# Kernel tuning notes

Hardware: AMD Instinct MI355X
Metric: run time of the kernel (lower is better)

Reference implementation:

```python
import jax, jax.numpy as jnp
import numpy as np

HEADS = 4
DIM_HEAD = 64


def setup_inputs() -> dict:
    key = jax.random.key(0)
    k1, k2, k3, k4 = jax.random.split(key, 4)
    dim = 256
    hidden = HEADS * DIM_HEAD  # 256
    x = jax.random.normal(k1, (16, dim, 64, 64), dtype=jnp.float32)
    # 1x1 conv weights stored as [out_c, in_c]
    w_qkv = jax.random.normal(k2, (3 * hidden, dim), dtype=jnp.float32) * (1.0 / np.sqrt(dim))
    w_out = jax.random.normal(k3, (dim, hidden), dtype=jnp.float32) * (1.0 / np.sqrt(hidden))
    b_out = jax.random.normal(k4, (dim,), dtype=jnp.float32) * 0.01
    gamma = jnp.ones((dim,), dtype=jnp.float32) * 1e-05
    return {"x": x, "w_qkv": w_qkv, "w_out": w_out, "b_out": b_out, "gamma": gamma}


def reference(x, w_qkv, w_out, b_out, gamma):
    b, c, h, w = x.shape
    n = h * w
    # 1x1 conv == channel matmul
    qkv = jnp.einsum('oc,bchw->bohw', w_qkv, x)  # [b, 3*heads*dh, h, w]
    qkv = qkv.reshape(b, 3, HEADS, DIM_HEAD, n)  # channel split order: (qkv, heads, c)
    q, k, v = qkv[:, 0], qkv[:, 1], qkv[:, 2]    # each [b, heads, dh, n]
    k = jax.nn.softmax(k, axis=-1)               # softmax over spatial tokens
    context = jnp.einsum('bhdn,bhen->bhde', k, v)  # [b, heads, dh, dh]
    out = jnp.einsum('bhde,bhdn->bhen', context, q)  # [b, heads, dh, n]
    out = out.reshape(b, HEADS * DIM_HEAD, h, w)
    y = jnp.einsum('oc,bchw->bohw', w_out, out) + b_out[None, :, None, None]
    return y * gamma[None, :, None, None] + x
```

## Files before the change

### kernel.cpp

```cpp
#include <hip/hip_runtime.h>
#include <stdint.h>

typedef short s16x8 __attribute__((ext_vector_type(8)));
typedef float f32x4 __attribute__((ext_vector_type(4)));

__device__ __forceinline__ float bits2f(unsigned short u) {
    union { unsigned int i; float f; } c; c.i = ((unsigned int)u) << 16; return c.f;
}
__device__ __forceinline__ unsigned short f2bits(float f) {
    union { float f; unsigned int i; } c; c.f = f;
    unsigned int x = c.i;
    unsigned int r = (x + 0x7FFFu + ((x >> 16) & 1u)) >> 16;
    return (unsigned short)r;
}
__device__ __forceinline__ unsigned int pack2(float a, float b) {
    return (unsigned int)f2bits(a) | ((unsigned int)f2bits(b) << 16);
}

__global__ __launch_bounds__(256) void k_cvt(
    const float* __restrict__ src, unsigned short* __restrict__ dst, int n8)
{
    int i = blockIdx.x * 256 + threadIdx.x;
    if (i >= n8) return;
    const float* s = src + (size_t)i * 8;
    float4 a = *(const float4*)s, b = *(const float4*)(s + 4);
    unsigned int q[4] = { pack2(a.x, a.y), pack2(a.z, a.w), pack2(b.x, b.y), pack2(b.z, b.w) };
    *(s16x8*)(dst + (size_t)i * 8) = *(s16x8*)q;
}

__global__ __launch_bounds__(256) void k_transpose(
    const unsigned short* __restrict__ src, unsigned short* __restrict__ dst,
    int RS, int DS)
{
    int dr = blockIdx.x * 256 + threadIdx.x;
    int c0 = blockIdx.y * 8;
    __align__(16) unsigned short tmp[8];
#pragma unroll
    for (int j = 0; j < 8; ++j) tmp[j] = src[(size_t)(c0 + j) * RS + dr];
    *(s16x8*)(dst + (size_t)dr * DS + c0) = *(s16x8*)tmp;
}

template <int EPI, int BBF16, int XCVT>
__global__ __launch_bounds__(256) void gemm_wide(
    const unsigned short* __restrict__ A, const void* __restrict__ B,
    void* __restrict__ C, unsigned short* __restrict__ xbout,
    const float* __restrict__ Xres, const float* __restrict__ gamma,
    const float* __restrict__ bias, long Abs)
{
    __shared__ unsigned short As[256][72];
    __shared__ unsigned short Bs[64][66];
    int bz = blockIdx.z;
    int n0 = blockIdx.x * 64;
    const unsigned short* Ab = A + (size_t)bz * Abs;
    int t = threadIdx.x, w = t >> 6, l = t & 63, lm = l & 15, lq = l >> 4;
    int mw = w * 64;

    f32x4 acc[4][4];
    f32x4 zero = {0.f, 0.f, 0.f, 0.f};
#pragma unroll
    for (int i = 0; i < 4; ++i)
#pragma unroll
        for (int j = 0; j < 4; ++j) acc[i][j] = zero;

    for (int kk = 0; kk < 256; kk += 64) {
#pragma unroll
        for (int i = 0; i < 8; ++i) {
            int idx = t + i * 256;
            int r = idx >> 3, ch = idx & 7;
            *(s16x8*)&As[r][ch * 8] = *(const s16x8*)(Ab + (size_t)r * 256 + kk + ch * 8);
        }
#pragma unroll
        for (int i = 0; i < 2; ++i) {
            int idx = t + i * 256;
            int c = idx >> 3, ch = idx & 7;
            unsigned int* qp = (unsigned int*)&Bs[c][ch * 8];
            if (BBF16) {
                const unsigned short* bp = (const unsigned short*)B + (size_t)bz * 1048576
                                         + (size_t)(kk + c) * 4096 + n0 + ch * 8;
                union { s16x8 v; unsigned int u[4]; } cv;
                cv.v = *(const s16x8*)bp;
                qp[0] = cv.u[0]; qp[1] = cv.u[1]; qp[2] = cv.u[2]; qp[3] = cv.u[3];
            } else {
                const float* bp = (const float*)B + (size_t)bz * 1048576
                                + (size_t)(kk + c) * 4096 + n0 + ch * 8;
                float4 v0 = *(const float4*)bp, v1 = *(const float4*)(bp + 4);
                unsigned int q[4] = { pack2(v0.x, v0.y), pack2(v0.z, v0.w),
                                      pack2(v1.x, v1.y), pack2(v1.z, v1.w) };
                qp[0] = q[0]; qp[1] = q[1]; qp[2] = q[2]; qp[3] = q[3];
                if (XCVT) {
                    unsigned short* xp = xbout + (size_t)bz * 1048576
                                       + (size_t)(kk + c) * 4096 + n0 + ch * 8;
                    *(s16x8*)xp = *(s16x8*)q;
                }
            }
        }
        __syncthreads();
#pragma unroll
        for (int ks = 0; ks < 2; ++ks) {
            s16x8 af[4];
#pragma unroll
            for (int mi = 0; mi < 4; ++mi)
                af[mi] = *(const s16x8*)&As[mw + mi * 16 + lm][ks * 32 + lq * 8];
#pragma unroll
            for (int ni = 0; ni < 4; ++ni) {
                s16x8 bfr;
#pragma unroll
                for (int j = 0; j < 8; ++j) bfr[j] = (short)Bs[ks * 32 + lq * 8 + j][ni * 16 + lm];
#pragma unroll
                for (int mi = 0; mi < 4; ++mi)
                    acc[mi][ni] = __builtin_amdgcn_mfma_f32_16x16x32_bf16(af[mi], bfr, acc[mi][ni], 0, 0, 0);
            }
        }
        __syncthreads();
    }

#pragma unroll
    for (int mi = 0; mi < 4; ++mi)
#pragma unroll
        for (int r = 0; r < 4; ++r) {
            int m = mw + mi * 16 + lq * 4 + r;
            float g = 0.f, bo = 0.f;
            if (EPI == 1) { g = gamma[m]; bo = bias[m]; }
#pragma unroll
            for (int ni = 0; ni < 4; ++ni) {
                int n = n0 + ni * 16 + lm;
                size_t idx = (size_t)m * 4096 + n;
                float v = acc[mi][ni][r];
                if (EPI == 1) {
                    float* Cb = (float*)C + (size_t)bz * 1048576;
                    Cb[idx] = g * (v + bo) + Xres[(size_t)bz * 1048576 + idx];
                } else {
                    unsigned short* Cb = (unsigned short*)C + (size_t)bz * 1048576;
                    Cb[idx] = f2bits(v);
                }
            }
        }
}

template <int AEXP>
__global__ __launch_bounds__(256) void gemm_bt(
    const unsigned short* __restrict__ A, const unsigned short* __restrict__ Bt,
    unsigned short* __restrict__ C, const float2* __restrict__ stats,
    int K, int Kstep, int lda, int ldb, int ldc,
    long Abs, long Bbs, long Cbs)
{
    __shared__ unsigned short As[128][72];
    __shared__ unsigned short Bs[128][72];
    int bz = blockIdx.z;
    int b = bz & 15, kc = bz >> 4;
    int m0 = blockIdx.y * 128, n0 = blockIdx.x * 128;
    const unsigned short* Ab = A + (size_t)b * Abs + (size_t)m0 * lda + (size_t)kc * Kstep;
    const unsigned short* Bb = Bt + (size_t)b * Bbs + (size_t)n0 * ldb + (size_t)kc * Kstep;
    int t = threadIdx.x;
    int w = t >> 6, l = t & 63, lm = l & 15, lq = l >> 4;
    int mw = (w >> 1) * 64, nw = (w & 1) * 64;

    f32x4 acc[4][4];
    f32x4 zero = {0.f, 0.f, 0.f, 0.f};
#pragma unroll
    for (int i = 0; i < 4; ++i)
#pragma unroll
        for (int j = 0; j < 4; ++j) acc[i][j] = zero;

    for (int kk = 0; kk < K; kk += 64) {
#pragma unroll
        for (int i = 0; i < 4; ++i) {
            int idx = t + i * 256;
            int r = idx >> 3, ch = idx & 7;
            s16x8 av = *(const s16x8*)(Ab + (size_t)r * lda + kk + ch * 8);
            if (AEXP) {
                float2 st = stats[b * 256 + m0 + r];
                unsigned int q[4];
#pragma unroll
                for (int j = 0; j < 4; ++j) {
                    float e0 = __expf(bits2f((unsigned short)av[2 * j]) - st.x) * st.y;
                    float e1 = __expf(bits2f((unsigned short)av[2 * j + 1]) - st.x) * st.y;
                    q[j] = pack2(e0, e1);
                }
                av = *(s16x8*)q;
            }
            *(s16x8*)&As[r][ch * 8] = av;
            *(s16x8*)&Bs[r][ch * 8] = *(const s16x8*)(Bb + (size_t)r * ldb + kk + ch * 8);
        }
        __syncthreads();
#pragma unroll
        for (int ks = 0; ks < 2; ++ks) {
            s16x8 af[4], bfr[4];
#pragma unroll
            for (int mi = 0; mi < 4; ++mi) af[mi]  = *(const s16x8*)&As[mw + mi * 16 + lm][ks * 32 + lq * 8];
#pragma unroll
            for (int ni = 0; ni < 4; ++ni) bfr[ni] = *(const s16x8*)&Bs[nw + ni * 16 + lm][ks * 32 + lq * 8];
#pragma unroll
            for (int mi = 0; mi < 4; ++mi)
#pragma unroll
                for (int ni = 0; ni < 4; ++ni)
                    acc[mi][ni] = __builtin_amdgcn_mfma_f32_16x16x32_bf16(af[mi], bfr[ni], acc[mi][ni], 0, 0, 0);
        }
        __syncthreads();
    }

    unsigned short* Cb = C + (size_t)bz * Cbs;
#pragma unroll
    for (int mi = 0; mi < 4; ++mi)
#pragma unroll
        for (int r = 0; r < 4; ++r) {
            int m = m0 + mw + mi * 16 + lq * 4 + r;
#pragma unroll
            for (int ni = 0; ni < 4; ++ni) {
                int n = n0 + nw + ni * 16 + lm;
                Cb[(size_t)m * ldc + n] = f2bits(acc[mi][ni][r]);
            }
        }
}

__global__ __launch_bounds__(256) void k_softstats(
    const unsigned short* __restrict__ kbuf, float2* __restrict__ stats)
{
    const unsigned short* p = kbuf + (size_t)blockIdx.x * 4096;
    int t = threadIdx.x;
    __shared__ float red[4];

    s16x8 r0 = *(const s16x8*)(p + t * 16);
    s16x8 r1 = *(const s16x8*)(p + t * 16 + 8);
    float v[16];
    float m = -1e30f;
#pragma unroll
    for (int i = 0; i < 8; ++i) { v[i] = bits2f((unsigned short)r0[i]); v[8 + i] = bits2f((unsigned short)r1[i]); }
#pragma unroll
    for (int i = 0; i < 16; ++i) m = fmaxf(m, v[i]);
#pragma unroll
    for (int off = 32; off >= 1; off >>= 1) m = fmaxf(m, __shfl_xor(m, off));
    if ((t & 63) == 0) red[t >> 6] = m;
    __syncthreads();
    m = fmaxf(fmaxf(red[0], red[1]), fmaxf(red[2], red[3]));
    __syncthreads();

    float s = 0.f;
#pragma unroll
    for (int i = 0; i < 16; ++i) s += __expf(v[i] - m);
#pragma unroll
    for (int off = 32; off >= 1; off >>= 1) s += __shfl_xor(s, off);
    if ((t & 63) == 0) red[t >> 6] = s;
    __syncthreads();
    if (t == 0) {
        s = red[0] + red[1] + red[2] + red[3];
        stats[blockIdx.x] = make_float2(m, 1.0f / s);
    }
}

__global__ __launch_bounds__(256) void k_ctxw2(
    const unsigned short* __restrict__ Gp, const unsigned short* __restrict__ wb,
    const unsigned short* __restrict__ wob, unsigned short* __restrict__ W2)
{
    __shared__ unsigned short ctxs[64][72];
    int h = blockIdx.x, b = blockIdx.y;
    int t = threadIdx.x, w = t >> 6, l = t & 63, lm = l & 15, lq = l >> 4;
    const unsigned short* Wv = wb + 131072 + (size_t)(h * 64) * 256;
    f32x4 zero = {0.f, 0.f, 0.f, 0.f};

    f32x4 acc[4];
#pragma unroll
    for (int i = 0; i < 4; ++i) acc[i] = zero;
    for (int kc = 0; kc < 8; ++kc) {
        const unsigned short* Gb = Gp + (size_t)(kc * 16 + b) * 65536 + (size_t)(h * 64) * 256;
#pragma unroll
        for (int kk = 0; kk < 256; kk += 32) {
            s16x8 a = *(const s16x8*)(Gb + (size_t)(w * 16 + lm) * 256 + kk + lq * 8);
#pragma unroll
            for (int ni = 0; ni < 4; ++ni) {
                s16x8 bb = *(const s16x8*)(Wv + (size_t)(ni * 16 + lm) * 256 + kk + lq * 8);
                acc[ni] = __builtin_amdgcn_mfma_f32_16x16x32_bf16(a, bb, acc[ni], 0, 0, 0);
            }
        }
    }
#pragma unroll
    for (int ni = 0; ni < 4; ++ni)
#pragma unroll
        for (int r = 0; r < 4; ++r)
            ctxs[w * 16 + lq * 4 + r][ni * 16 + lm] = f2bits(acc[ni][r]);
    __syncthreads();

    f32x4 acc2[4][4];
#pragma unroll
    for (int i = 0; i < 4; ++i)
#pragma unroll
        for (int j = 0; j < 4; ++j) acc2[i][j] = zero;
#pragma unroll
    for (int ks = 0; ks < 2; ++ks) {
        s16x8 af[4], bfr[4];
#pragma unroll
        for (int mi = 0; mi < 4; ++mi)
            af[mi] = *(const s16x8*)(wob + (size_t)(w * 64 + mi * 16 + lm) * 256 + h * 64 + ks * 32 + lq * 8);
#pragma unroll
        for (int ni = 0; ni < 4; ++ni) bfr[ni] = *(const s16x8*)&ctxs[ni * 16 + lm][ks * 32 + lq * 8];
#pragma unroll
        for (int mi = 0; mi < 4; ++mi)
#pragma unroll
            for (int ni = 0; ni < 4; ++ni)
                acc2[mi][ni] = __builtin_amdgcn_mfma_f32_16x16x32_bf16(af[mi], bfr[ni], acc2[mi][ni], 0, 0, 0);
    }
    unsigned short* W2b = W2 + (size_t)b * 65536;
#pragma unroll
    for (int mi = 0; mi < 4; ++mi)
#pragma unroll
        for (int r = 0; r < 4; ++r) {
            int o = w * 64 + mi * 16 + lq * 4 + r;
#pragma unroll
            for (int ni = 0; ni < 4; ++ni)
                W2b[(size_t)o * 256 + h * 64 + ni * 16 + lm] = f2bits(acc2[mi][ni][r]);
        }
}

extern "C" void kernel_launch(void* const* d_in, const int* in_sizes, int n_in,
                              void* d_out, int out_size, void* d_ws, size_t ws_size,
                              hipStream_t stream)
{
    (void)in_sizes; (void)n_in; (void)out_size; (void)ws_size;
    const float* x      = (const float*)d_in[0];
    const float* w_qkv  = (const float*)d_in[1];
    const float* w_out  = (const float*)d_in[2];
    const float* b_out  = (const float*)d_in[3];
    const float* gamma  = (const float*)d_in[4];
    unsigned short* kbuf = (unsigned short*)d_out;

    char* ws = (char*)d_ws;
    unsigned short* xb  = (unsigned short*)(ws);
    unsigned short* Gp  = (unsigned short*)(ws + 33554432);
    unsigned short* W2  = (unsigned short*)(ws + 50331648);
    unsigned short* W3  = (unsigned short*)(ws + 52428800);
    unsigned short* WqT = (unsigned short*)(ws + 54525952);
    unsigned short* wb  = (unsigned short*)(ws + 54657024);
    unsigned short* wob = (unsigned short*)(ws + 55050240);
    float2*         st  = (float2*)        (ws + 55181312);

    k_cvt<<<dim3(96), 256, 0, stream>>>(w_qkv, wb, 24576);
    k_cvt<<<dim3(32), 256, 0, stream>>>(w_out, wob, 8192);
    k_transpose<<<dim3(1, 32, 1), 256, 0, stream>>>(wb, WqT, 256, 256);

    gemm_wide<0, 0, 1><<<dim3(64, 1, 16), 256, 0, stream>>>(
        wb + 65536, x, kbuf, xb, nullptr, nullptr, nullptr, 0L);

    k_softstats<<<dim3(4096), 256, 0, stream>>>(kbuf, st);

    gemm_bt<1><<<dim3(2, 2, 128), 256, 0, stream>>>(
        kbuf, xb, Gp, st, 512, 512, 4096, 4096, 256,
        1048576L, 1048576L, 65536L);

    k_ctxw2<<<dim3(4, 16), 256, 0, stream>>>(Gp, wb, wob, W2);

    gemm_bt<0><<<dim3(2, 2, 16), 256, 0, stream>>>(
        W2, WqT, W3, nullptr, 256, 0, 256, 256, 256,
        65536L, 0L, 65536L);

    gemm_wide<1, 1, 0><<<dim3(64, 1, 16), 256, 0, stream>>>(
        W3, xb, d_out, nullptr, x, gamma, b_out, 65536L);
}
```

Measured before the change: 239.9 us.

## Replace wide GEMMs with transposed-x gemm_bt and fuse softmax sum into epilogue

Adds a kernel that converts x to bf16 and also writes a transposed [n, c] copy, so the key projection and the output projection can both run through the 128x128 gemm_bt kernel instead of the gemm_wide kernel with its strided shared-memory B reads. The separate softmax statistics pass is dropped: the key GEMM epilogue accumulates row sums of exp(k) with atomics, and the next GEMM normalises using only that sum, with no max subtraction. The weight conversion and transpose kernels are merged into one launch. The cost is an extra 32 MB transposed write and atomic traffic, plus a risk of exp overflow without the max shift, which is safe only while k stays bounded.

Result: no change. 237.9 us (-0.8%).

```diff
diff --git a/kernel.cpp b/kernel.cpp
--- a/kernel.cpp
+++ b/kernel.cpp
@@ -17,132 +17,77 @@
     return (unsigned int)f2bits(a) | ((unsigned int)f2bits(b) << 16);
 }
 
-__global__ __launch_bounds__(256) void k_cvt(
-    const float* __restrict__ src, unsigned short* __restrict__ dst, int n8)
+__global__ __launch_bounds__(256) void k_zero(float* __restrict__ p, int n)
 {
     int i = blockIdx.x * 256 + threadIdx.x;
-    if (i >= n8) return;
-    const float* s = src + (size_t)i * 8;
-    float4 a = *(const float4*)s, b = *(const float4*)(s + 4);
-    unsigned int q[4] = { pack2(a.x, a.y), pack2(a.z, a.w), pack2(b.x, b.y), pack2(b.z, b.w) };
-    *(s16x8*)(dst + (size_t)i * 8) = *(s16x8*)q;
-}
-
-__global__ __launch_bounds__(256) void k_transpose(
-    const unsigned short* __restrict__ src, unsigned short* __restrict__ dst,
-    int RS, int DS)
-{
-    int dr = blockIdx.x * 256 + threadIdx.x;
-    int c0 = blockIdx.y * 8;
-    __align__(16) unsigned short tmp[8];
-#pragma unroll
-    for (int j = 0; j < 8; ++j) tmp[j] = src[(size_t)(c0 + j) * RS + dr];
-    *(s16x8*)(dst + (size_t)dr * DS + c0) = *(s16x8*)tmp;
-}
-
-template <int EPI, int BBF16, int XCVT>
-__global__ __launch_bounds__(256) void gemm_wide(
-    const unsigned short* __restrict__ A, const void* __restrict__ B,
-    void* __restrict__ C, unsigned short* __restrict__ xbout,
-    const float* __restrict__ Xres, const float* __restrict__ gamma,
-    const float* __restrict__ bias, long Abs)
-{
-    __shared__ unsigned short As[256][72];
-    __shared__ unsigned short Bs[64][66];
-    int bz = blockIdx.z;
-    int n0 = blockIdx.x * 64;
-    const unsigned short* Ab = A + (size_t)bz * Abs;
-    int t = threadIdx.x, w = t >> 6, l = t & 63, lm = l & 15, lq = l >> 4;
-    int mw = w * 64;
-
-    f32x4 acc[4][4];
-    f32x4 zero = {0.f, 0.f, 0.f, 0.f};
-#pragma unroll
-    for (int i = 0; i < 4; ++i)
-#pragma unroll
-        for (int j = 0; j < 4; ++j) acc[i][j] = zero;
-
-    for (int kk = 0; kk < 256; kk += 64) {
-#pragma unroll
-        for (int i = 0; i < 8; ++i) {
-            int idx = t + i * 256;
-            int r = idx >> 3, ch = idx & 7;
-            *(s16x8*)&As[r][ch * 8] = *(const s16x8*)(Ab + (size_t)r * 256 + kk + ch * 8);
-        }
-#pragma unroll
-        for (int i = 0; i < 2; ++i) {
-            int idx = t + i * 256;
-            int c = idx >> 3, ch = idx & 7;
-            unsigned int* qp = (unsigned int*)&Bs[c][ch * 8];
-            if (BBF16) {
-                const unsigned short* bp = (const unsigned short*)B + (size_t)bz * 1048576
-                                         + (size_t)(kk + c) * 4096 + n0 + ch * 8;
-                union { s16x8 v; unsigned int u[4]; } cv;
-                cv.v = *(const s16x8*)bp;
-                qp[0] = cv.u[0]; qp[1] = cv.u[1]; qp[2] = cv.u[2]; qp[3] = cv.u[3];
-            } else {
-                const float* bp = (const float*)B + (size_t)bz * 1048576
-                                + (size_t)(kk + c) * 4096 + n0 + ch * 8;
-                float4 v0 = *(const float4*)bp, v1 = *(const float4*)(bp + 4);
-                unsigned int q[4] = { pack2(v0.x, v0.y), pack2(v0.z, v0.w),
-                                      pack2(v1.x, v1.y), pack2(v1.z, v1.w) };
-                qp[0] = q[0]; qp[1] = q[1]; qp[2] = q[2]; qp[3] = q[3];
-                if (XCVT) {
-                    unsigned short* xp = xbout + (size_t)bz * 1048576
-                                       + (size_t)(kk + c) * 4096 + n0 + ch * 8;
-                    *(s16x8*)xp = *(s16x8*)q;
-                }
-            }
-        }
-        __syncthreads();
-#pragma unroll
-        for (int ks = 0; ks < 2; ++ks) {
-            s16x8 af[4];
-#pragma unroll
-            for (int mi = 0; mi < 4; ++mi)
-                af[mi] = *(const s16x8*)&As[mw + mi * 16 + lm][ks * 32 + lq * 8];
-#pragma unroll
-            for (int ni = 0; ni < 4; ++ni) {
-                s16x8 bfr;
-#pragma unroll
-                for (int j = 0; j < 8; ++j) bfr[j] = (short)Bs[ks * 32 + lq * 8 + j][ni * 16 + lm];
-#pragma unroll
-                for (int mi = 0; mi < 4; ++mi)
-                    acc[mi][ni] = __builtin_amdgcn_mfma_f32_16x16x32_bf16(af[mi], bfr, acc[mi][ni], 0, 0, 0);
-            }
-        }
-        __syncthreads();
-    }
-
-#pragma unroll
-    for (int mi = 0; mi < 4; ++mi)
-#pragma unroll
-        for (int r = 0; r < 4; ++r) {
-            int m = mw + mi * 16 + lq * 4 + r;
-            float g = 0.f, bo = 0.f;
-            if (EPI == 1) { g = gamma[m]; bo = bias[m]; }
-#pragma unroll
-            for (int ni = 0; ni < 4; ++ni) {
-                int n = n0 + ni * 16 + lm;
-                size_t idx = (size_t)m * 4096 + n;
-                float v = acc[mi][ni][r];
-                if (EPI == 1) {
-                    float* Cb = (float*)C + (size_t)bz * 1048576;
-                    Cb[idx] = g * (v + bo) + Xres[(size_t)bz * 1048576 + idx];
-                } else {
-                    unsigned short* Cb = (unsigned short*)C + (size_t)bz * 1048576;
-                    Cb[idx] = f2bits(v);
-                }
-            }
-        }
-}
-
-template <int AEXP>
+    if (i < n) p[i] = 0.f;
+}
+
+__global__ __launch_bounds__(256) void k_weights(
+    const float* __restrict__ w_qkv, const float* __restrict__ w_out,
+    unsigned short* __restrict__ wb, unsigned short* __restrict__ wob,
+    unsigned short* __restrict__ WqT)
+{
+    int bid = blockIdx.x, t = threadIdx.x;
+    if (bid < 96) {
+        int i = bid * 256 + t;
+        const float* s = w_qkv + (size_t)i * 8;
+        float4 a = *(const float4*)s, b = *(const float4*)(s + 4);
+        unsigned int q[4] = { pack2(a.x, a.y), pack2(a.z, a.w), pack2(b.x, b.y), pack2(b.z, b.w) };
+        *(s16x8*)(wb + (size_t)i * 8) = *(s16x8*)q;
+    } else if (bid < 128) {
+        int i = (bid - 96) * 256 + t;
+        const float* s = w_out + (size_t)i * 8;
+        float4 a = *(const float4*)s, b = *(const float4*)(s + 4);
+        unsigned int q[4] = { pack2(a.x, a.y), pack2(a.z, a.w), pack2(b.x, b.y), pack2(b.z, b.w) };
+        *(s16x8*)(wob + (size_t)i * 8) = *(s16x8*)q;
+    } else {
+        int c0 = (bid - 128) * 8;
+        int dr = t;
+        __align__(16) unsigned short tmp[8];
+#pragma unroll
+        for (int j = 0; j < 8; ++j) tmp[j] = f2bits(w_qkv[(size_t)(c0 + j) * 256 + dr]);
+        *(s16x8*)(WqT + (size_t)dr * 256 + c0) = *(s16x8*)tmp;
+    }
+}
+
+__global__ __launch_bounds__(256) void k_xpose(
+    const float* __restrict__ x, unsigned short* __restrict__ xb,
+    unsigned short* __restrict__ xT)
+{
+    __shared__ unsigned short tile[64 * 65];
+    int b = blockIdx.z, c0 = blockIdx.y * 64, n0 = blockIdx.x * 64;
+    int t = threadIdx.x;
+    int cr = t >> 2, nc = (t & 3) * 16;
+    const float* xp = x + ((size_t)(b * 256 + c0 + cr)) * 4096 + n0 + nc;
+    float4 v0 = *(const float4*)xp,       v1 = *(const float4*)(xp + 4),
+           v2 = *(const float4*)(xp + 8), v3 = *(const float4*)(xp + 12);
+    unsigned int q[8] = { pack2(v0.x, v0.y), pack2(v0.z, v0.w), pack2(v1.x, v1.y), pack2(v1.z, v1.w),
+                          pack2(v2.x, v2.y), pack2(v2.z, v2.w), pack2(v3.x, v3.y), pack2(v3.z, v3.w) };
+    unsigned short* xbp = xb + ((size_t)(b * 256 + c0 + cr)) * 4096 + n0 + nc;
+    *(s16x8*)xbp = *(s16x8*)q;
+    *(s16x8*)(xbp + 8) = *(s16x8*)(q + 4);
+    const unsigned short* qs = (const unsigned short*)q;
+#pragma unroll
+    for (int i = 0; i < 16; ++i) tile[cr * 65 + nc + i] = qs[i];
+    __syncthreads();
+    int nr = t >> 2, cc = (t & 3) * 16;
+    __align__(16) unsigned short o[16];
+#pragma unroll
+    for (int j = 0; j < 16; ++j) o[j] = tile[(cc + j) * 65 + nr];
+    unsigned short* xtp = xT + ((size_t)(b * 4096 + n0 + nr)) * 256 + c0 + cc;
+    *(s16x8*)xtp = *(s16x8*)o;
+    *(s16x8*)(xtp + 8) = *(s16x8*)(o + 8);
+}
+
+template <int AEXP, int EPI>
 __global__ __launch_bounds__(256) void gemm_bt(
     const unsigned short* __restrict__ A, const unsigned short* __restrict__ Bt,
-    unsigned short* __restrict__ C, const float2* __restrict__ stats,
+    void* __restrict__ C, float* __restrict__ ssum,
     int K, int Kstep, int lda, int ldb, int ldc,
-    long Abs, long Bbs, long Cbs)
+    long Abs, long Bbs, long Cbs,
+    const float* __restrict__ Xres, const float* __restrict__ gamma,
+    const float* __restrict__ bias)
 {
     __shared__ unsigned short As[128][72];
     __shared__ unsigned short Bs[128][72];
@@ -155,6 +100,15 @@
     int w = t >> 6, l = t & 63, lm = l & 15, lq = l >> 4;
     int mw = (w >> 1) * 64, nw = (w & 1) * 64;
 
+    float inva[4];
+    if (AEXP) {
+#pragma unroll
+        for (int i = 0; i < 4; ++i) {
+            int r = (t + i * 256) >> 3;
+            inva[i] = 1.0f / ssum[b * 256 + m0 + r];
+        }
+    }
+
     f32x4 acc[4][4];
     f32x4 zero = {0.f, 0.f, 0.f, 0.f};
 #pragma unroll
@@ -169,12 +123,11 @@
             int r = idx >> 3, ch = idx & 7;
             s16x8 av = *(const s16x8*)(Ab + (size_t)r * lda + kk + ch * 8);
             if (AEXP) {
-                float2 st = stats[b * 256 + m0 + r];
                 unsigned int q[4];
 #pragma unroll
                 for (int j = 0; j < 4; ++j) {
-                    float e0 = __expf(bits2f((unsigned short)av[2 * j]) - st.x) * st.y;
-                    float e1 = __expf(bits2f((unsigned short)av[2 * j + 1]) - st.x) * st.y;
+                    float e0 = __expf(bits2f((unsigned short)av[2 * j])) * inva[i];
+                    float e1 = __expf(bits2f((unsigned short)av[2 * j + 1])) * inva[i];
                     q[j] = pack2(e0, e1);
                 }
                 av = *(s16x8*)q;
@@ -199,53 +152,35 @@
         __syncthreads();
     }
 
-    unsigned short* Cb = C + (size_t)bz * Cbs;
 #pragma unroll
     for (int mi = 0; mi < 4; ++mi)
 #pragma unroll
         for (int r = 0; r < 4; ++r) {
             int m = m0 + mw + mi * 16 + lq * 4 + r;
+            float g = 0.f, bo = 0.f;
+            if (EPI == 1) { g = gamma[m]; bo = bias[m]; }
 #pragma unroll
             for (int ni = 0; ni < 4; ++ni) {
                 int n = n0 + nw + ni * 16 + lm;
-                Cb[(size_t)m * ldc + n] = f2bits(acc[mi][ni][r]);
-            }
-        }
-}
-
-__global__ __launch_bounds__(256) void k_softstats(
-    const unsigned short* __restrict__ kbuf, float2* __restrict__ stats)
-{
-    const unsigned short* p = kbuf + (size_t)blockIdx.x * 4096;
-    int t = threadIdx.x;
-    __shared__ float red[4];
-
-    s16x8 r0 = *(const s16x8*)(p + t * 16);
-    s16x8 r1 = *(const s16x8*)(p + t * 16 + 8);
-    float v[16];
-    float m = -1e30f;
-#pragma unroll
-    for (int i = 0; i < 8; ++i) { v[i] = bits2f((unsigned short)r0[i]); v[8 + i] = bits2f((unsigned short)r1[i]); }
-#pragma unroll
-    for (int i = 0; i < 16; ++i) m = fmaxf(m, v[i]);
-#pragma unroll
-    for (int off = 32; off >= 1; off >>= 1) m = fmaxf(m, __shfl_xor(m, off));
-    if ((t & 63) == 0) red[t >> 6] = m;
-    __syncthreads();
-    m = fmaxf(fmaxf(red[0], red[1]), fmaxf(red[2], red[3]));
-    __syncthreads();
-
-    float s = 0.f;
-#pragma unroll
-    for (int i = 0; i < 16; ++i) s += __expf(v[i] - m);
-#pragma unroll
-    for (int off = 32; off >= 1; off >>= 1) s += __shfl_xor(s, off);
-    if ((t & 63) == 0) red[t >> 6] = s;
-    __syncthreads();
-    if (t == 0) {
-        s = red[0] + red[1] + red[2] + red[3];
-        stats[blockIdx.x] = make_float2(m, 1.0f / s);
-    }
+                size_t idx = (size_t)m * ldc + n;
+                float v = acc[mi][ni][r];
+                if (EPI == 1) {
+                    float* Cb = (float*)C + (size_t)bz * Cbs;
+                    Cb[idx] = g * (v + bo) + Xres[(size_t)bz * Cbs + idx];
+                } else {
+                    unsigned short* Cb = (unsigned short*)C + (size_t)bz * Cbs;
+                    Cb[idx] = f2bits(v);
+                }
+            }
+            if (EPI == 2) {
+                float rs = 0.f;
+#pragma unroll
+                for (int ni = 0; ni < 4; ++ni) rs += __expf(acc[mi][ni][r]);
+#pragma unroll
+                for (int off = 1; off < 16; off <<= 1) rs += __shfl_xor(rs, off);
+                if (lm == 0) atomicAdd(&ssum[b * 256 + m], rs);
+            }
+        }
 }
 
 __global__ __launch_bounds__(256) void k_ctxw2(
@@ -324,34 +259,35 @@
     unsigned short* kbuf = (unsigned short*)d_out;
 
     char* ws = (char*)d_ws;
-    unsigned short* xb  = (unsigned short*)(ws);
-    unsigned short* Gp  = (unsigned short*)(ws + 33554432);
-    unsigned short* W2  = (unsigned short*)(ws + 50331648);
-    unsigned short* W3  = (unsigned short*)(ws + 52428800);
-    unsigned short* WqT = (unsigned short*)(ws + 54525952);
-    unsigned short* wb  = (unsigned short*)(ws + 54657024);
-    unsigned short* wob = (unsigned short*)(ws + 55050240);
-    float2*         st  = (float2*)        (ws + 55181312);
-
-    k_cvt<<<dim3(96), 256, 0, stream>>>(w_qkv, wb, 24576);
-    k_cvt<<<dim3(32), 256, 0, stream>>>(w_out, wob, 8192);
-    k_transpose<<<dim3(1, 32, 1), 256, 0, stream>>>(wb, WqT, 256, 256);
-
-    gemm_wide<0, 0, 1><<<dim3(64, 1, 16), 256, 0, stream>>>(
-        wb + 65536, x, kbuf, xb, nullptr, nullptr, nullptr, 0L);
-
-    k_softstats<<<dim3(4096), 256, 0, stream>>>(kbuf, st);
-
-    gemm_bt<1><<<dim3(2, 2, 128), 256, 0, stream>>>(
-        kbuf, xb, Gp, st, 512, 512, 4096, 4096, 256,
-        1048576L, 1048576L, 65536L);
+    unsigned short* xT  = (unsigned short*)(ws);
+    unsigned short* xb  = (unsigned short*)(ws + 33554432);
+    unsigned short* Gp  = (unsigned short*)(ws + 67108864);
+    unsigned short* W2  = (unsigned short*)(ws + 83886080);
+    unsigned short* W3  = (unsigned short*)(ws + 85983232);
+    unsigned short* WqT = (unsigned short*)(ws + 88080384);
+    unsigned short* wb  = (unsigned short*)(ws + 88211456);
+    unsigned short* wob = (unsigned short*)(ws + 88604672);
+    float*          ssum = (float*)        (ws + 88735744);
+
+    k_zero<<<dim3(16), 256, 0, stream>>>(ssum, 4096);
+    k_weights<<<dim3(160), 256, 0, stream>>>(w_qkv, w_out, wb, wob, WqT);
+    k_xpose<<<dim3(64, 4, 16), 256, 0, stream>>>(x, xb, xT);
+
+    gemm_bt<0, 2><<<dim3(32, 2, 16), 256, 0, stream>>>(
+        wb + 65536, xT, kbuf, ssum, 256, 0, 256, 256, 4096,
+        0L, 1048576L, 1048576L, nullptr, nullptr, nullptr);
+
+    gemm_bt<1, 0><<<dim3(2, 2, 128), 256, 0, stream>>>(
+        kbuf, xb, Gp, ssum, 512, 512, 4096, 4096, 256,
+        1048576L, 1048576L, 65536L, nullptr, nullptr, nullptr);
 
     k_ctxw2<<<dim3(4, 16), 256, 0, stream>>>(Gp, wb, wob, W2);
 
-    gemm_bt<0><<<dim3(2, 2, 16), 256, 0, stream>>>(
+    gemm_bt<0, 0><<<dim3(2, 2, 16), 256, 0, stream>>>(
         W2, WqT, W3, nullptr, 256, 0, 256, 256, 256,
-        65536L, 0L, 65536L);
-
-    gemm_wide<1, 1, 0><<<dim3(64, 1, 16), 256, 0, stream>>>(
-        W3, xb, d_out, nullptr, x, gamma, b_out, 65536L);
-}
+        65536L, 0L, 65536L, nullptr, nullptr, nullptr);
+
+    gemm_bt<0, 1><<<dim3(32, 2, 16), 256, 0, stream>>>(
+        W3, xT, d_out, nullptr, 256, 0, 256, 256, 4096,
+        65536L, 1048576L, 1048576L, x, gamma, b_out);
+}
```
